# Kernel tuning notes

Hardware: AMD Instinct MI355X
Metric: run time of the kernel (lower is better)

Reference implementation:

```python
import jax, jax.numpy as jnp
import numpy as np

N_NODES = 100000


def _graph_conv(x, W, b, src, dst, inv_sqrt_out, inv_sqrt_in):
    # DGL GraphConv, norm='both':  D_in^{-1/2} A D_out^{-1/2} X W + b
    h = x * inv_sqrt_out[:, None]
    if W.shape[0] > W.shape[1]:
        # in_feats > out_feats: transform first (cheaper aggregation)
        h = h @ W
        m = jax.ops.segment_sum(h[src], dst, num_segments=N_NODES)
    else:
        m = jax.ops.segment_sum(h[src], dst, num_segments=N_NODES)
        m = m @ W
    return m * inv_sqrt_in[:, None] + b


def _degree_norms(src, dst):
    ones = jnp.ones(src.shape[0], dtype=jnp.float32)
    out_deg = jax.ops.segment_sum(ones, src, num_segments=N_NODES)
    in_deg = jax.ops.segment_sum(ones, dst, num_segments=N_NODES)
    # DGL clamps degree to min 1 (allow_zero_in_degree)
    return jnp.clip(out_deg, 1.0) ** -0.5, jnp.clip(in_deg, 1.0) ** -0.5


def setup_inputs() -> dict:
    key = jax.random.key(0)
    ks = jax.random.split(key, 8)
    E = 800000
    in_feats, h1, h2, nc = 128, 256, 128, 40
    return {
        "features": jax.random.normal(ks[0], (N_NODES, in_feats), dtype=jnp.float32),
        "src": jax.random.randint(ks[1], (E,), 0, N_NODES),
        "dst": jax.random.randint(ks[2], (E,), 0, N_NODES),
        "W1": jax.random.normal(ks[3], (in_feats, h1), dtype=jnp.float32) * (2.0 / (in_feats + h1)) ** 0.5,
        "b1": jnp.zeros((h1,), dtype=jnp.float32),
        "W2": jax.random.normal(ks[4], (h1, h2), dtype=jnp.float32) * (2.0 / (h1 + h2)) ** 0.5,
        "b2": jnp.zeros((h2,), dtype=jnp.float32),
        "W3": jax.random.normal(ks[5], (h2, nc), dtype=jnp.float32) * (2.0 / (h2 + nc)) ** 0.5,
        "b3": jnp.zeros((nc,), dtype=jnp.float32),
    }


def reference(features, src, dst, W1, b1, W2, b2, W3, b3):
    inv_out, inv_in = _degree_norms(src, dst)
    h = _graph_conv(features, W1, b1, src, dst, inv_out, inv_in)
    h = jax.nn.relu(h)
    h = _graph_conv(h, W2, b2, src, dst, inv_out, inv_in)
    h = jax.nn.relu(h)
    return _graph_conv(h, W3, b3, src, dst, inv_out, inv_in)
```

## Files before the change

### kernel.cpp

```cpp
#include <hip/hip_runtime.h>

#define N_NODES 100000
#define SCAN_NB 128
#define SCAN_TPB 256
#define GCOUNT 8
#define BINS 12500
#define NSLICE 32

typedef _Float16 half_t;
typedef __attribute__((ext_vector_type(8))) _Float16 v8h;
typedef __attribute__((ext_vector_type(4))) _Float16 v4h;
typedef __attribute__((ext_vector_type(4))) float v4f;


__global__ __launch_bounds__(512) void hist_all(
    const int* __restrict__ src, const int* __restrict__ dst,
    int* __restrict__ loc, unsigned short* __restrict__ partialI,
    unsigned short* __restrict__ partialO, int E,
    const float* __restrict__ W1, const float* __restrict__ W2,
    const float* __restrict__ W3, half_t* __restrict__ Wt1,
    half_t* __restrict__ Wt2, half_t* __restrict__ Wt3) {
    __shared__ int hist[BINS];
    const int bid = blockIdx.x;
    const int tid = threadIdx.x;
    if (bid < 2 * GCOUNT * NSLICE) {
        const bool isDst = bid < GCOUNT * NSLICE;
        const int b2 = isDst ? bid : bid - GCOUNT * NSLICE;
        const int g = b2 >> 5, s = b2 & (NSLICE - 1);
        const int gbase = g * BINS;
        for (int b = tid; b < BINS; b += 512) hist[b] = 0;
        __syncthreads();
        const int chunk = (E + NSLICE - 1) / NSLICE;
        const int e0 = s * chunk;
        const int e1 = min(e0 + chunk, E);
        if (isDst) {
            for (int e = e0 + tid; e < e1; e += 512) {
                int d = dst[e];
                unsigned lb = (unsigned)(d - gbase);
                if (lb < (unsigned)BINS) loc[e] = atomicAdd(&hist[lb], 1);
            }
        } else {
            for (int e = e0 + tid; e < e1; e += 512) {
                int d = src[e];
                unsigned lb = (unsigned)(d - gbase);
                if (lb < (unsigned)BINS) atomicAdd(&hist[lb], 1);
            }
        }
        __syncthreads();
        unsigned short* p = (isDst ? partialI : partialO) + (size_t)b2 * BINS;
        for (int b = tid; b < BINS; b += 512) p[b] = (unsigned short)hist[b];
    } else {
        int u = (bid - 2 * GCOUNT * NSLICE) * 512 + tid;
        if (u < 32768) {
            int n = u >> 7, k = u & 127;
            Wt1[u] = (half_t)W1[(size_t)k * 256 + n];
        } else if (u < 65536) {
            int w = u - 32768;
            int n = w >> 8, k = w & 255;
            Wt2[w] = (half_t)W2[(size_t)k * 128 + n];
        } else if (u < 70656) {
            int w = u - 65536;
            int n = w >> 7, k = w & 127;
            Wt3[w] = (half_t)W3[(size_t)k * 40 + n];
        }
    }
}


__global__ __launch_bounds__(SCAN_TPB) void scan_reduce(
    const unsigned short* __restrict__ partialI, int* __restrict__ blockSum, int n) {
    __shared__ int s[SCAN_TPB];
    int chunk = (n + SCAN_NB - 1) / SCAN_NB;
    int beg = blockIdx.x * chunk;
    int end = min(beg + chunk, n);
    int sum = 0;
    for (int i = beg + threadIdx.x; i < end; i += SCAN_TPB) {
        int g = i / BINS, lb = i - g * BINS;
        const unsigned short* p = partialI + (size_t)g * NSLICE * BINS + lb;
#pragma unroll
        for (int sl = 0; sl < NSLICE; ++sl) sum += p[(size_t)sl * BINS];
    }
    s[threadIdx.x] = sum;
    __syncthreads();
    for (int off = SCAN_TPB / 2; off > 0; off >>= 1) {
        if (threadIdx.x < off) s[threadIdx.x] += s[threadIdx.x + off];
        __syncthreads();
    }
    if (threadIdx.x == 0) blockSum[blockIdx.x] = s[0];
}

__global__ __launch_bounds__(SCAN_NB) void scan_offsets(int* __restrict__ blockSum,
                                                        int* __restrict__ rowptr_total) {
    __shared__ int s[SCAN_NB];
    int tid = threadIdx.x;
    int v = blockSum[tid];
    s[tid] = v;
    __syncthreads();
    for (int off = 1; off < SCAN_NB; off <<= 1) {
        int t = (tid >= off) ? s[tid - off] : 0;
        __syncthreads();
        s[tid] += t;
        __syncthreads();
    }
    blockSum[tid] = s[tid] - v;
    if (tid == SCAN_NB - 1) rowptr_total[0] = s[tid];
}

__global__ __launch_bounds__(SCAN_TPB) void scan_final(
    unsigned short* __restrict__ partialI, const unsigned short* __restrict__ partialO,
    const int* __restrict__ blockSum, int* __restrict__ rowptr,
    float* __restrict__ invIn, float* __restrict__ invOut, int n) {
    __shared__ int s[SCAN_TPB];
    int chunk = (n + SCAN_NB - 1) / SCAN_NB;
    int beg = blockIdx.x * chunk;
    int end = min(beg + chunk, n);
    int carry = blockSum[blockIdx.x];
    for (int base = beg; base < end; base += SCAN_TPB) {
        int i = base + threadIdx.x;
        int v = 0, o = 0;
        if (i < end) {
            int g = i / BINS, lb = i - g * BINS;
            unsigned short* p = partialI + (size_t)g * NSLICE * BINS + lb;
            int run = 0;
#pragma unroll
            for (int sl = 0; sl < NSLICE; ++sl) {
                int c = p[(size_t)sl * BINS];
                p[(size_t)sl * BINS] = (unsigned short)run;
                run += c;
            }
            v = run;
            const unsigned short* q = partialO + (size_t)g * NSLICE * BINS + lb;
#pragma unroll
            for (int sl = 0; sl < NSLICE; ++sl) o += q[(size_t)sl * BINS];
        }
        s[threadIdx.x] = v;
        __syncthreads();
        for (int off = 1; off < SCAN_TPB; off <<= 1) {
            int t = (threadIdx.x >= off) ? s[threadIdx.x - off] : 0;
            __syncthreads();
            s[threadIdx.x] += t;
            __syncthreads();
        }
        int excl = s[threadIdx.x] - v;
        if (i < end) {
            rowptr[i] = carry + excl;
            invOut[i] = rsqrtf((float)max(o, 1));
            invIn[i] = rsqrtf((float)max(v, 1));
        }
        int roundSum = s[SCAN_TPB - 1];
        __syncthreads();
        carry += roundSum;
    }
}


__global__ void prep2(const int* __restrict__ src, const int* __restrict__ dst,
                      const int* __restrict__ loc,
                      const unsigned short* __restrict__ partialI,
                      const int* __restrict__ rowptr,
                      int* __restrict__ eidx, int E,
                      const float* __restrict__ x, const float* __restrict__ invOut,
                      half_t* __restrict__ xh) {
    int t = blockIdx.x * blockDim.x + threadIdx.x;
    if (t < E) {
        int d = dst[t];
        int chunk = (E + NSLICE - 1) / NSLICE;
        int s = t / chunk;
        int g = d / BINS, lb = d - g * BINS;
        int pre = partialI[(size_t)(g * NSLICE + s) * BINS + lb];
        eidx[rowptr[d] + pre + loc[t]] = src[t];
    } else {
        int u = t - E;
        if (u < N_NODES * 32) {
            int n = u >> 5;
            float4 v = ((const float4*)x)[u];
            float s = invOut[n];
            v4h h;
            h[0] = (half_t)(v.x * s);
            h[1] = (half_t)(v.y * s);
            h[2] = (half_t)(v.z * s);
            h[3] = (half_t)(v.w * s);
            *(v4h*)(xh + (size_t)u * 4) = h;
        }
    }
}


template <int F>
__device__ __forceinline__ void gather_row(const half_t* __restrict__ x,
                                           const int* __restrict__ eidx,
                                           int beg, int end, int c, float* acc) {
    const half_t* __restrict__ xc = x + (size_t)c * 8;
    int n = end - beg;
    if (n <= 0) return;
    int nbat = (n + 3) >> 2;
    int i0 = eidx[beg];
    int i1 = eidx[beg + min(1, n - 1)];
    int i2 = eidx[beg + min(2, n - 1)];
    int i3 = eidx[beg + min(3, n - 1)];
    for (int b = 0; b < nbat; ++b) {
        int j = b * 4;
        v8h v0 = *(const v8h*)(xc + (size_t)i0 * F);
        v8h v1 = *(const v8h*)(xc + (size_t)i1 * F);
        v8h v2 = *(const v8h*)(xc + (size_t)i2 * F);
        v8h v3 = *(const v8h*)(xc + (size_t)i3 * F);
        if (b + 1 < nbat) {
            int jn = j + 4;
            i0 = eidx[beg + jn];
            i1 = eidx[beg + min(jn + 1, n - 1)];
            i2 = eidx[beg + min(jn + 2, n - 1)];
            i3 = eidx[beg + min(jn + 3, n - 1)];
        }
        v8h z = (v8h)(half_t)0;
        v1 = (j + 1 < n) ? v1 : z;
        v2 = (j + 2 < n) ? v2 : z;
        v3 = (j + 3 < n) ? v3 : z;
#pragma unroll
        for (int q = 0; q < 8; ++q)
            acc[q] += ((float)v0[q] + (float)v1[q]) + ((float)v2[q] + (float)v3[q]);
    }
}


__global__ __launch_bounds__(256, 8) void gather1(
    const half_t* __restrict__ xh, const int* __restrict__ rowptr,
    const int* __restrict__ eidx, half_t* __restrict__ A1) {
    int t = blockIdx.x * 256 + threadIdx.x;
    int n = t >> 4, c = t & 15;
    if (n >= N_NODES) return;
    float acc[8] = {};
    gather_row<128>(xh, eidx, rowptr[n], rowptr[n + 1], c, acc);
    v8h o;
#pragma unroll
    for (int q = 0; q < 8; ++q) o[q] = (half_t)acc[q];
    *(v8h*)(A1 + (size_t)n * 128 + c * 8) = o;
}


__global__ __launch_bounds__(512) void gather2t3(
    const half_t* __restrict__ t2, const int* __restrict__ rowptr,
    const int* __restrict__ eidx, const float* __restrict__ invIn,
    const float* __restrict__ invOut, const float* __restrict__ b2,
    const half_t* __restrict__ Wt3, half_t* __restrict__ t3) {
    constexpr int K = 128, N = 40, LDA = K + 8;
    __shared__ half_t As[32][LDA];
    const int tid = threadIdx.x;
    const int wave = tid >> 6, lane = tid & 63;
    const int quad = lane >> 4, l16 = lane & 15;
    const int m0 = blockIdx.x * 32;
    const int mt = wave & 1, jn = wave >> 1;

    v8h b[4];
    if (jn < 3) {
        int gn = jn * 16 + l16;
#pragma unroll
        for (int kc = 0; kc < 4; ++kc)
            b[kc] = (gn < N) ? *(const v8h*)(Wt3 + (size_t)gn * K + kc * 32 + quad * 8)
                             : (v8h)(half_t)0;
    }

    {
        int r = tid >> 4, c = tid & 15;
        int n = m0 + r;
        float acc[8] = {};
        float ii = 0.f, io = 0.f;
        if (n < N_NODES) {
            ii = invIn[n];
            io = invOut[n];
            gather_row<128>(t2, eidx, rowptr[n], rowptr[n + 1], c, acc);
        }
        float4 blo = ((const float4*)b2)[c * 2];
        float4 bhi = ((const float4*)b2)[c * 2 + 1];
        float bb[8] = {blo.x, blo.y, blo.z, blo.w, bhi.x, bhi.y, bhi.z, bhi.w};
        v8h o;
#pragma unroll
        for (int q = 0; q < 8; ++q)
            o[q] = (half_t)fmaxf((acc[q] * ii + bb[q]) * io, 0.f);
        *(v8h*)&As[r][c * 8] = o;
    }
    __syncthreads();

    if (jn < 3) {
        v8h a[4];
#pragma unroll
        for (int kc = 0; kc < 4; ++kc)
            a[kc] = *(const v8h*)&As[mt * 16 + l16][kc * 32 + quad * 8];
        v4f acc = {};
#pragma unroll
        for (int kc = 0; kc < 4; ++kc)
            acc = __builtin_amdgcn_mfma_f32_16x16x32_f16(a[kc], b[kc], acc, 0, 0, 0);
        int gn = jn * 16 + l16;
        if (gn < N) {
#pragma unroll
            for (int r = 0; r < 4; ++r) {
                int gm = m0 + mt * 16 + quad * 4 + r;
                if (gm < N_NODES) t3[(size_t)gm * N + gn] = (half_t)acc[r];
            }
        }
    }
}


__global__ __launch_bounds__(512) void mlp12(
    const half_t* __restrict__ A1, const half_t* __restrict__ Wt1,
    const half_t* __restrict__ Wt2,
    const float* __restrict__ invIn, const float* __restrict__ invOut,
    const float* __restrict__ b1, half_t* __restrict__ t2) {
    constexpr int K1 = 128, K2 = 256, N2 = 128;
    constexpr int LDA = K1 + 8;
    constexpr int LDH = K2 + 8;
    __shared__ half_t As[64][LDA];
    __shared__ half_t h1S[64][LDH];
    __shared__ float iiS[64], ioS[64];
    const int tid = threadIdx.x;
    const int wave = tid >> 6, lane = tid & 63;
    const int quad = lane >> 4, l16 = lane & 15;
    const int m0 = blockIdx.x * 64;
    const int n0 = wave * 32;

    v8h b[2][4];
    float bv[2];
#pragma unroll
    for (int j = 0; j < 2; ++j) {
        int gn = n0 + j * 16 + l16;
        bv[j] = b1[gn];
#pragma unroll
        for (int kc = 0; kc < 4; ++kc)
            b[j][kc] = *(const v8h*)(Wt1 + (size_t)gn * K1 + kc * 32 + quad * 8);
    }
    if (tid < 64) {
        int gm = m0 + tid;
        bool ok = gm < N_NODES;
        iiS[tid] = ok ? invIn[gm] : 0.f;
        ioS[tid] = ok ? invOut[gm] : 0.f;
    }

#pragma unroll
    for (int p = 0; p < 2; ++p) {
        int task = tid + p * 512;
        int r = task >> 4, c = task & 15;
        int gm = m0 + r;
        v8h v = (gm < N_NODES) ? *(const v8h*)(A1 + (size_t)gm * K1 + c * 8)
                               : (v8h)(half_t)0;
        *(v8h*)&As[r][c * 8] = v;
    }
    __syncthreads();

    for (int mt = 0; mt < 4; ++mt) {
        v8h a[4];
#pragma unroll
        for (int kc = 0; kc < 4; ++kc)
            a[kc] = *(const v8h*)&As[mt * 16 + l16][kc * 32 + quad * 8];
        v4f acc[2] = {};
#pragma unroll
        for (int kc = 0; kc < 4; ++kc)
#pragma unroll
            for (int j = 0; j < 2; ++j)
                acc[j] = __builtin_amdgcn_mfma_f32_16x16x32_f16(a[kc], b[j][kc], acc[j], 0, 0, 0);
#pragma unroll
        for (int j = 0; j < 2; ++j) {
            int cn = n0 + j * 16 + l16;
#pragma unroll
            for (int r = 0; r < 4; ++r) {
                int lr = mt * 16 + quad * 4 + r;
                float z = (acc[j][r] * iiS[lr] + bv[j]) * ioS[lr];
                h1S[lr][cn] = (half_t)fmaxf(z, 0.f);
            }
        }
    }

    v8h b2[8];
    const int n02 = wave * 16;
    {
        int gn = n02 + l16;
#pragma unroll
        for (int kc = 0; kc < 8; ++kc)
            b2[kc] = *(const v8h*)(Wt2 + (size_t)gn * K2 + kc * 32 + quad * 8);
    }
    __syncthreads();

    for (int mt = 0; mt < 4; ++mt) {
        v8h a2[8];
#pragma unroll
        for (int kc = 0; kc < 8; ++kc)
            a2[kc] = *(const v8h*)&h1S[mt * 16 + l16][kc * 32 + quad * 8];
        v4f acc2 = {};
#pragma unroll
        for (int kc = 0; kc < 8; ++kc)
            acc2 = __builtin_amdgcn_mfma_f32_16x16x32_f16(a2[kc], b2[kc], acc2, 0, 0, 0);
        int gn = n02 + l16;
#pragma unroll
        for (int r = 0; r < 4; ++r) {
            int gm = m0 + mt * 16 + quad * 4 + r;
            if (gm < N_NODES) t2[(size_t)gm * N2 + gn] = (half_t)acc2[r];
        }
    }
}


__global__ __launch_bounds__(256, 8) void gather_final(
    const half_t* __restrict__ x,
    const int* __restrict__ rowptr, const int* __restrict__ eidx,
    float* __restrict__ out, const float* __restrict__ invIn,
    const float* __restrict__ bias) {
    constexpr int F = 40, V = 5;
    int t = blockIdx.x * blockDim.x + threadIdx.x;
    int n = t / V;
    int v = t - n * V;
    if (n >= N_NODES) return;
    float acc[8] = {};
    gather_row<F>(x, eidx, rowptr[n], rowptr[n + 1], v, acc);
    float ii = invIn[n];
    float* o = out + (size_t)n * F + v * 8;
#pragma unroll
    for (int q = 0; q < 8; ++q) o[q] = acc[q] * ii + bias[v * 8 + q];
}


extern "C" void kernel_launch(void* const* d_in, const int* in_sizes, int n_in,
                              void* d_out, int out_size, void* d_ws, size_t ws_size,
                              hipStream_t stream) {
    const float* x  = (const float*)d_in[0];
    const int* src  = (const int*)d_in[1];
    const int* dst  = (const int*)d_in[2];
    const float* W1 = (const float*)d_in[3];
    const float* b1 = (const float*)d_in[4];
    const float* W2 = (const float*)d_in[5];
    const float* b2 = (const float*)d_in[6];
    const float* W3 = (const float*)d_in[7];
    const float* b3 = (const float*)d_in[8];
    float* out = (float*)d_out;
    const int E = in_sizes[1];

    char* ws = (char*)d_ws;
    float* inv_out = (float*)ws;
    float* inv_in  = (float*)(ws + 400000);
    int* rowptr    = (int*)(ws + 800000);
    int* eidx      = (int*)(ws + 1600256);
    int* blockSum  = (int*)(ws + 4800256);
    half_t* Wt1    = (half_t*)(ws + 4800768);
    half_t* Wt2    = (half_t*)(ws + 4866304);
    half_t* Wt3    = (half_t*)(ws + 4931840);
    half_t* bufA   = (half_t*)(ws + 5000192);
    half_t* bufB   = (half_t*)(ws + 30600192);
    int* loc = (int*)bufB;
    unsigned short* partialI = (unsigned short*)((char*)bufB + 3200000);
    unsigned short* partialO = partialI + (size_t)GCOUNT * NSLICE * BINS;

    const int NBH = 2 * GCOUNT * NSLICE + (70656 + 511) / 512;
    hist_all<<<NBH, 512, 0, stream>>>(src, dst, loc, partialI, partialO, E,
                                      W1, W2, W3, Wt1, Wt2, Wt3);
    scan_reduce<<<SCAN_NB, SCAN_TPB, 0, stream>>>(partialI, blockSum, N_NODES);
    scan_offsets<<<1, SCAN_NB, 0, stream>>>(blockSum, rowptr + N_NODES);
    scan_final<<<SCAN_NB, SCAN_TPB, 0, stream>>>(partialI, partialO, blockSum, rowptr,
                                                 inv_in, inv_out, N_NODES);
    prep2<<<(E + N_NODES * 32 + 255) / 256, 256, 0, stream>>>(src, dst, loc, partialI,
                                                              rowptr, eidx, E,
                                                              x, inv_out, bufA);

    const int NBG = (N_NODES * 16 + 255) / 256;
    const int NB  = (N_NODES + 63) / 64;
    const int NBF = (N_NODES + 31) / 32;

    gather1<<<NBG, 256, 0, stream>>>(bufA, rowptr, eidx, bufB);
    mlp12<<<NB, 512, 0, stream>>>(bufB, Wt1, Wt2, inv_in, inv_out, b1, bufA);
    gather2t3<<<NBF, 512, 0, stream>>>(bufA, rowptr, eidx, inv_in, inv_out, b2, Wt3, bufB);
    gather_final<<<(N_NODES * 5 + 255) / 256, 256, 0, stream>>>(
        bufB, rowptr, eidx, out, inv_in, b3);
}
```

Baseline: 283.4 us.

## Pre-bucket edges by source range before CSR build to improve gather locality

Adds a three-kernel counting sort (count, scan, scatter) that partitions edges into 32 source-node ranges before the histogram and CSR construction. Within each destination row, edges become ordered by source range, so later neighbor gathers touch node features in a more clustered pattern, which should improve cache hit rates. The cost is three extra launches and an extra read and write pass over the edge arrays, plus relocated workspace buffers that must not overlap.

```diff
diff --git a/kernel.cpp b/kernel.cpp
--- a/kernel.cpp
+++ b/kernel.cpp
@@ -6,11 +6,67 @@
 #define GCOUNT 8
 #define BINS 12500
 #define NSLICE 32
+#define NRANGE 32
+#define NBK 256
 
 typedef _Float16 half_t;
 typedef __attribute__((ext_vector_type(8))) _Float16 v8h;
 typedef __attribute__((ext_vector_type(4))) _Float16 v4h;
 typedef __attribute__((ext_vector_type(4))) float v4f;
+
+
+__global__ __launch_bounds__(512) void bucket_count(
+    const int* __restrict__ src, int* __restrict__ loc2,
+    int* __restrict__ partialB, int E) {
+    __shared__ int cnt[NRANGE];
+    const int tid = threadIdx.x, bid = blockIdx.x;
+    if (tid < NRANGE) cnt[tid] = 0;
+    __syncthreads();
+    int ch = (E + NBK - 1) / NBK;
+    int e0 = bid * ch, e1 = min(e0 + ch, E);
+    for (int e = e0 + tid; e < e1; e += 512) {
+        int r = src[e] / (N_NODES / NRANGE);
+        loc2[e] = atomicAdd(&cnt[r], 1);
+    }
+    __syncthreads();
+    if (tid < NRANGE) partialB[tid * NBK + bid] = cnt[tid];
+}
+
+__global__ __launch_bounds__(512) void bucket_scan(int* __restrict__ partialB) {
+    __shared__ int s[512];
+    const int tid = threadIdx.x;
+    int vals[16];
+    int sum = 0;
+#pragma unroll
+    for (int k = 0; k < 16; ++k) { vals[k] = partialB[tid * 16 + k]; sum += vals[k]; }
+    s[tid] = sum;
+    __syncthreads();
+    for (int off = 1; off < 512; off <<= 1) {
+        int t = (tid >= off) ? s[tid - off] : 0;
+        __syncthreads();
+        s[tid] += t;
+        __syncthreads();
+    }
+    int excl = s[tid] - sum;
+#pragma unroll
+    for (int k = 0; k < 16; ++k) { partialB[tid * 16 + k] = excl; excl += vals[k]; }
+}
+
+__global__ __launch_bounds__(512) void bucket_scatter(
+    const int* __restrict__ src, const int* __restrict__ dst,
+    const int* __restrict__ loc2, const int* __restrict__ partialB,
+    int* __restrict__ srcP, int* __restrict__ dstP, int E) {
+    const int tid = threadIdx.x, bid = blockIdx.x;
+    int ch = (E + NBK - 1) / NBK;
+    int e0 = bid * ch, e1 = min(e0 + ch, E);
+    for (int e = e0 + tid; e < e1; e += 512) {
+        int sv = src[e];
+        int r = sv / (N_NODES / NRANGE);
+        int np = partialB[r * NBK + bid] + loc2[e];
+        srcP[np] = sv;
+        dstP[np] = dst[e];
+    }
+}
 
 
 __global__ __launch_bounds__(512) void hist_all(
@@ -436,6 +492,7 @@
     float* inv_out = (float*)ws;
     float* inv_in  = (float*)(ws + 400000);
     int* rowptr    = (int*)(ws + 800000);
+    int* partialB  = (int*)(ws + 1200256);
     int* eidx      = (int*)(ws + 1600256);
     int* blockSum  = (int*)(ws + 4800256);
     half_t* Wt1    = (half_t*)(ws + 4800768);
@@ -445,16 +502,23 @@
     half_t* bufB   = (half_t*)(ws + 30600192);
     int* loc = (int*)bufB;
     unsigned short* partialI = (unsigned short*)((char*)bufB + 3200000);
-    unsigned short* partialO = partialI + (size_t)GCOUNT * NSLICE * BINS;
+    unsigned short* partialO = (unsigned short*)((char*)bufB + 9600000);
+    int* srcP = (int*)((char*)bufB + 16000000);
+    int* dstP = (int*)((char*)bufB + 19200000);
+    int* loc2 = (int*)((char*)bufB + 22400000);
+
+    bucket_count<<<NBK, 512, 0, stream>>>(src, loc2, partialB, E);
+    bucket_scan<<<1, 512, 0, stream>>>(partialB);
+    bucket_scatter<<<NBK, 512, 0, stream>>>(src, dst, loc2, partialB, srcP, dstP, E);
 
     const int NBH = 2 * GCOUNT * NSLICE + (70656 + 511) / 512;
-    hist_all<<<NBH, 512, 0, stream>>>(src, dst, loc, partialI, partialO, E,
+    hist_all<<<NBH, 512, 0, stream>>>(srcP, dstP, loc, partialI, partialO, E,
                                       W1, W2, W3, Wt1, Wt2, Wt3);
     scan_reduce<<<SCAN_NB, SCAN_TPB, 0, stream>>>(partialI, blockSum, N_NODES);
     scan_offsets<<<1, SCAN_NB, 0, stream>>>(blockSum, rowptr + N_NODES);
     scan_final<<<SCAN_NB, SCAN_TPB, 0, stream>>>(partialI, partialO, blockSum, rowptr,
                                                  inv_in, inv_out, N_NODES);
-    prep2<<<(E + N_NODES * 32 + 255) / 256, 256, 0, stream>>>(src, dst, loc, partialI,
+    prep2<<<(E + N_NODES * 32 + 255) / 256, 256, 0, stream>>>(srcP, dstP, loc, partialI,
                                                               rowptr, eidx, E,
                                                               x, inv_out, bufA);
 
```

Result: slower. 297.9 us (+5.1%).
